# Kernel tuning notes

Hardware: AMD Instinct MI355X
Metric: run time of the kernel (lower is better)

Reference implementation:

```python
import jax, jax.numpy as jnp
import numpy as np

N_SRC, N_DST, DEG = 100000, 50000, 16
NODE_IN, EDGE_IN, HID = 128, 64, 64
E = N_DST * DEG


def sparsemax(z):
    # z: [..., K]; sparsemax along last axis (Martins & Astudillo)
    z = z - jnp.max(z, axis=-1, keepdims=True)
    zs = -jnp.sort(-z, axis=-1)  # descending sort
    k_range = jnp.arange(1, z.shape[-1] + 1, dtype=z.dtype)
    cs = jnp.cumsum(zs, axis=-1)
    is_gt = (1.0 + k_range * zs > cs).astype(z.dtype)
    k = jnp.max(is_gt * k_range, axis=-1, keepdims=True)
    tau = (jnp.sum(is_gt * zs, axis=-1, keepdims=True) - 1.0) / k
    return jnp.maximum(z - tau, 0.0)


def setup_inputs() -> dict:
    key = jax.random.key(0)
    ks = jax.random.split(key, 8)
    s = 0.02
    return {
        "node_features": jax.random.normal(ks[0], (N_SRC, NODE_IN), jnp.float32),
        "edge_features": jax.random.normal(ks[1], (E, EDGE_IN), jnp.float32),
        "src_idx": jax.random.randint(ks[2], (E,), 0, N_SRC, jnp.int32),
        "We": s * jax.random.normal(ks[3], (EDGE_IN, HID), jnp.float32),
        "be": jnp.zeros((HID,), jnp.float32),
        "Wa": s * jax.random.normal(ks[4], (EDGE_IN, HID), jnp.float32),
        "ba": jnp.zeros((HID,), jnp.float32),
        "wa": s * jax.random.normal(ks[5], (HID,), jnp.float32),
        "Wo": s * jax.random.normal(ks[6], (NODE_IN + HID, HID), jnp.float32),
        "bo": jnp.zeros((HID,), jnp.float32),
        "Wn": s * jax.random.normal(ks[7], (NODE_IN + HID, HID), jnp.float32),
        "bn": jnp.zeros((HID,), jnp.float32),
        "n_dst": N_DST,
        "deg": DEG,
    }


def reference(node_features, edge_features, src_idx, We, be, Wa, ba, wa, Wo, bo, Wn, bn, n_dst, deg):
    # dropout is identity in eval / p=0
    h_dst = node_features[:n_dst]                               # [n_dst, node_in]
    # message_func: per-edge transforms
    e_out = jax.nn.relu(edge_features @ We + be)                # [E, hid]
    a = jax.nn.leaky_relu((edge_features @ Wa + ba) @ wa)       # [E]
    h_src_e = node_features[src_idx]                            # gather [E, node_in]
    m = jax.nn.relu(jnp.concatenate([h_src_e, e_out], axis=-1) @ Wo + bo)  # [E, hid]
    # reduce_func: mailbox is [n_dst, deg, .] (fixed in-degree graph)
    a = a.reshape(n_dst, deg)
    m = m.reshape(n_dst, deg, -1)
    alpha = sparsemax(a)                                        # [n_dst, deg]
    h_neigh = jnp.einsum('nd,ndh->nh', alpha, m)                # [n_dst, hid]
    # node update
    return jax.nn.relu(jnp.concatenate([h_dst, h_neigh], axis=-1) @ Wn + bn)
```

## Files before the change

### kernel.cpp

```cpp
#include <hip/hip_runtime.h>


#define ND 50000
#define NS 100000

typedef __bf16 bf16x8 __attribute__((ext_vector_type(8)));
typedef float f32x4 __attribute__((ext_vector_type(4)));
typedef unsigned short u16x4 __attribute__((ext_vector_type(4)));

__device__ __forceinline__ void sync_wave() {
  asm volatile("s_waitcnt lgkmcnt(0)" ::: "memory");
}

__device__ __forceinline__ unsigned short f2bf(float x) {
  unsigned u = __float_as_uint(x);
  u += 0x7fffu + ((u >> 16) & 1u);
  return (unsigned short)(u >> 16);
}
__device__ __forceinline__ float bf2f(unsigned short u) {
  return __uint_as_float((unsigned)u << 16);
}

union Frag8 { bf16x8 v; unsigned u32[4]; };

__device__ __forceinline__ bf16x8 pack8(const float* fr) {
  Frag8 f;
  #pragma unroll
  for (int j = 0; j < 4; ++j) {
    unsigned lo = __float_as_uint(fr[2 * j]) + 0x8000u;
    unsigned hi = __float_as_uint(fr[2 * j + 1]) + 0x8000u;
    f.u32[j] = __builtin_amdgcn_perm(hi, lo, 0x07060302);
  }
  return f.v;
}

#define MFMA(a, b, c) __builtin_amdgcn_mfma_f32_16x16x32_bf16((a), (b), (c), 0, 0, 0)

extern "C" __global__ void gteast_prep(const float* __restrict__ Wa,
                                       const float* __restrict__ ba,
                                       const float* __restrict__ wa,
                                       float* __restrict__ vc) {
  __shared__ float red[260];
  const int tid = threadIdx.x, k = tid >> 2, p = tid & 3;
  float s = 0.f;
  for (int h = 16 * p; h < 16 * p + 16; ++h) s += Wa[k * 64 + h] * wa[h];
  red[tid] = s;
  if (tid < 4) {
    float sc = 0.f;
    for (int h = 16 * tid; h < 16 * tid + 16; ++h) sc += ba[h] * wa[h];
    red[256 + tid] = sc;
  }
  __syncthreads();
  if (p == 0) vc[k] = red[4 * k] + red[4 * k + 1] + red[4 * k + 2] + red[4 * k + 3];
  if (tid == 0) vc[64] = red[256] + red[257] + red[258] + red[259];
}

extern "C" __global__ void __launch_bounds__(256, 3)
gteast_src(const float* __restrict__ nf, const float* __restrict__ Wo,
           const float* __restrict__ Wn,
           unsigned short* __restrict__ y, unsigned short* __restrict__ z) {
  __shared__ unsigned short WuT[64 * 136];
  __shared__ unsigned short WnuT[64 * 136];
  const int tid = threadIdx.x;
  for (int i = tid; i < 128 * 64; i += 256) {
    int k = i >> 6, n = i & 63;
    WuT[n * 136 + k] = f2bf(Wo[i]);
    WnuT[n * 136 + k] = f2bf(Wn[i]);
  }
  __syncthreads();

  const int lane = tid & 63, w = tid >> 6, q = lane >> 4, t = lane & 15;
  const int tile = blockIdx.x * 4 + w;
  if (tile >= NS / 16) return;
  const int r0 = tile * 16;

  float raw[8];
  bf16x8 af[4];
  const float* hp = nf + (long)(r0 + t) * 128 + q * 8;
  #pragma unroll
  for (int kc = 0; kc < 4; ++kc) {
    float4 a0 = *reinterpret_cast<const float4*>(hp + kc * 32);
    float4 a1 = *reinterpret_cast<const float4*>(hp + kc * 32 + 4);
    raw[0] = a0.x; raw[1] = a0.y; raw[2] = a0.z; raw[3] = a0.w;
    raw[4] = a1.x; raw[5] = a1.y; raw[6] = a1.z; raw[7] = a1.w;
    af[kc] = pack8(raw);
  }

  f32x4 accY[4];
  #pragma unroll
  for (int nt = 0; nt < 4; ++nt) {
    f32x4 c = {0.f, 0.f, 0.f, 0.f};
    #pragma unroll
    for (int kc = 0; kc < 4; ++kc)
      c = MFMA(af[kc], *reinterpret_cast<const bf16x8*>(&WuT[(nt * 16 + t) * 136 + kc * 32 + q * 8]), c);
    accY[nt] = c;
  }
  #pragma unroll
  for (int r = 0; r < 4; ++r) {
    u16x4 v = {f2bf(accY[0][r]), f2bf(accY[1][r]), f2bf(accY[2][r]), f2bf(accY[3][r])};
    *reinterpret_cast<u16x4*>(y + (long)(r0 + 4 * q + r) * 64 + t * 4) = v;
  }

  if (tile < ND / 16) {
    f32x4 accZ[4];
    #pragma unroll
    for (int nt = 0; nt < 4; ++nt) {
      f32x4 c = {0.f, 0.f, 0.f, 0.f};
      #pragma unroll
      for (int kc = 0; kc < 4; ++kc)
        c = MFMA(af[kc], *reinterpret_cast<const bf16x8*>(&WnuT[(nt * 16 + t) * 136 + kc * 32 + q * 8]), c);
      accZ[nt] = c;
    }
    #pragma unroll
    for (int r = 0; r < 4; ++r) {
      u16x4 v = {f2bf(accZ[0][r]), f2bf(accZ[1][r]), f2bf(accZ[2][r]), f2bf(accZ[3][r])};
      *reinterpret_cast<u16x4*>(z + (long)(r0 + 4 * q + r) * 64 + t * 4) = v;
    }
  }
}

extern "C" __global__ void __launch_bounds__(256, 3)
gteast_edge(const float* __restrict__ ef, const int* __restrict__ src_idx,
            const float* __restrict__ We, const float* __restrict__ be,
            const float* __restrict__ Wo, const float* __restrict__ bo,
            const float* __restrict__ vc, const unsigned short* __restrict__ y,
            float* __restrict__ hn_out) {
  __shared__ unsigned short WeT[64 * 72];
  __shared__ unsigned short WoLoT[64 * 72];
  __shared__ unsigned short Elds[4][16 * 72];
  __shared__ float vls[68];

  const int tid = threadIdx.x;
  for (int i = tid; i < 64 * 64; i += 256) {
    int k = i >> 6, n = i & 63;
    WeT[n * 72 + k] = f2bf(We[i]);
  }
  for (int i = tid; i < 64 * 64; i += 256) {
    int k = i >> 6, n = i & 63;
    WoLoT[n * 72 + k] = f2bf(Wo[(128 + k) * 64 + n]);
  }
  if (tid < 65) vls[tid] = vc[tid];
  __syncthreads();

  const int lane = tid & 63, w = tid >> 6;
  const int q = lane >> 4, t = lane & 15;
  const int wid = blockIdx.x * 4 + w;
  if (wid * 8 >= ND) return;

  unsigned short* E = Elds[w];
  const float cval = vls[64];
  float beL[4], boL[4];
  #pragma unroll
  for (int nt = 0; nt < 4; ++nt) { beL[nt] = be[nt * 16 + t]; boL[nt] = bo[nt * 16 + t]; }
  float vsl[16];
  #pragma unroll
  for (int j = 0; j < 8; ++j) { vsl[j] = vls[q * 8 + j]; vsl[8 + j] = vls[32 + q * 8 + j]; }

  const int si0 = src_idx[wid * 128 + lane];
  const int si1 = src_idx[wid * 128 + 64 + lane];

  const long ebase = (long)(wid * 128);

  float4 efn[4];
  {
    const float* er = ef + (ebase + t) * 64 + q * 8;
    efn[0] = *reinterpret_cast<const float4*>(er);
    efn[1] = *reinterpret_cast<const float4*>(er + 4);
    efn[2] = *reinterpret_cast<const float4*>(er + 32);
    efn[3] = *reinterpret_cast<const float4*>(er + 36);
  }
  u16x4 yv[4];
  #pragma unroll
  for (int r = 0; r < 4; ++r) {
    const int s0 = __shfl(si0, 4 * q + r);
    yv[r] = *reinterpret_cast<const u16x4*>(y + (long)s0 * 64 + t * 4);
  }

  for (int it = 0; it < 8; ++it) {
    const int n = wid * 8 + it;
    const int itn = it < 7 ? it + 1 : 7;

    float fe[16];
    fe[0] = efn[0].x; fe[1] = efn[0].y; fe[2] = efn[0].z; fe[3] = efn[0].w;
    fe[4] = efn[1].x; fe[5] = efn[1].y; fe[6] = efn[1].z; fe[7] = efn[1].w;
    fe[8] = efn[2].x; fe[9] = efn[2].y; fe[10] = efn[2].z; fe[11] = efn[2].w;
    fe[12] = efn[3].x; fe[13] = efn[3].y; fe[14] = efn[3].z; fe[15] = efn[3].w;
    {
      const float* er = ef + (ebase + itn * 16 + t) * 64 + q * 8;
      efn[0] = *reinterpret_cast<const float4*>(er);
      efn[1] = *reinterpret_cast<const float4*>(er + 4);
      efn[2] = *reinterpret_cast<const float4*>(er + 32);
      efn[3] = *reinterpret_cast<const float4*>(er + 36);
    }

    float ap = 0.f;
    #pragma unroll
    for (int j = 0; j < 16; ++j) ap += fe[j] * vsl[j];
    ap += __shfl_xor(ap, 16);
    ap += __shfl_xor(ap, 32);
    float a = ap + cval;
    a = a > 0.f ? a : 0.01f * a;

    const bf16x8 e0 = pack8(fe), e1 = pack8(fe + 8);
    #pragma unroll
    for (int nt = 0; nt < 4; ++nt) {
      f32x4 c = {0.f, 0.f, 0.f, 0.f};
      c = MFMA(e0, *reinterpret_cast<const bf16x8*>(&WeT[(nt * 16 + t) * 72 + q * 8]), c);
      c = MFMA(e1, *reinterpret_cast<const bf16x8*>(&WeT[(nt * 16 + t) * 72 + 32 + q * 8]), c);
      #pragma unroll
      for (int r = 0; r < 4; ++r) {
        float vv = fmaxf(c[r] + beL[nt], 0.f);
        E[(4 * q + r) * 72 + nt * 16 + t] = f2bf(vv);
      }
    }
    sync_wave();

    bf16x8 af4 = *reinterpret_cast<const bf16x8*>(&E[t * 72 + q * 8]);
    bf16x8 af5 = *reinterpret_cast<const bf16x8*>(&E[t * 72 + 32 + q * 8]);

    f32x4 accM[4];
    #pragma unroll
    for (int nt = 0; nt < 4; ++nt) {
      f32x4 c = {0.f, 0.f, 0.f, 0.f};
      c = MFMA(af4, *reinterpret_cast<const bf16x8*>(&WoLoT[(nt * 16 + t) * 72 + q * 8]), c);
      c = MFMA(af5, *reinterpret_cast<const bf16x8*>(&WoLoT[(nt * 16 + t) * 72 + 32 + q * 8]), c);
      #pragma unroll
      for (int r = 0; r < 4; ++r)
        c[r] = fmaxf(c[r] + bf2f(yv[r][nt]) + boL[nt], 0.f);
      accM[nt] = c;
    }
    sync_wave();

    #pragma unroll
    for (int r = 0; r < 4; ++r) {
      const int idx = 16 * itn + 4 * q + r;
      const int sn = (idx < 64) ? __shfl(si0, idx) : __shfl(si1, idx - 64);
      yv[r] = *reinterpret_cast<const u16x4*>(y + (long)sn * 64 + t * 4);
    }

    const float z = a;
    float cp = 0.f, sp = 0.f;
    #pragma unroll
    for (int r = 0; r < 4; ++r) {
      float zj = __shfl(z, 4 * q + r, 16);
      const bool ge = (zj >= z);
      cp += ge ? 1.f : 0.f;
      sp += ge ? zj : 0.f;
    }
    cp += __shfl_xor(cp, 16); sp += __shfl_xor(sp, 16);
    cp += __shfl_xor(cp, 32); sp += __shfl_xor(sp, 32);
    const bool valid = 1.f + cp * z > sp;
    float kf = valid ? cp : 0.f;
    float sv = valid ? sp : 0.f;
    #pragma unroll
    for (int m = 1; m < 16; m <<= 1) {
      float ok = __shfl_xor(kf, m), os = __shfl_xor(sv, m);
      if (ok > kf) { kf = ok; sv = os; }
    }
    const float tau = (sv - 1.f) / kf;
    const float alpha = fmaxf(a - tau, 0.f);

    float al[4];
    #pragma unroll
    for (int r = 0; r < 4; ++r) al[r] = __shfl(alpha, 4 * q + r);
    float p[4];
    #pragma unroll
    for (int nt = 0; nt < 4; ++nt) {
      p[nt] = al[0] * accM[nt][0] + al[1] * accM[nt][1] +
              al[2] * accM[nt][2] + al[3] * accM[nt][3];
      p[nt] += __shfl_xor(p[nt], 16);
      p[nt] += __shfl_xor(p[nt], 32);
    }
    const float pown = (q == 0) ? p[0] : (q == 1) ? p[1] : (q == 2) ? p[2] : p[3];
    hn_out[(long)n * 64 + lane] = pown;
  }
}

extern "C" __global__ void __launch_bounds__(256, 4)
gteast_out(const unsigned short* __restrict__ z, const float* __restrict__ Wn,
           const float* __restrict__ bn, float* __restrict__ out) {
  __shared__ unsigned short WnLoT[64 * 72];
  const int tid = threadIdx.x;
  for (int i = tid; i < 64 * 64; i += 256) {
    int k = i >> 6, nn = i & 63;
    WnLoT[nn * 72 + k] = f2bf(Wn[(128 + k) * 64 + nn]);
  }
  __syncthreads();

  const int lane = tid & 63, w = tid >> 6, q = lane >> 4, t = lane & 15;
  const int tile = blockIdx.x * 4 + w;
  if (tile >= ND / 16) return;
  const int r0 = tile * 16;

  float bnL[4];
  #pragma unroll
  for (int nt = 0; nt < 4; ++nt) bnL[nt] = bn[nt * 16 + t];

  float raw[8];
  bf16x8 af4, af5;
  const float* gp = out + (long)(r0 + t) * 64 + q * 8;
  {
    float4 a0 = *reinterpret_cast<const float4*>(gp);
    float4 a1 = *reinterpret_cast<const float4*>(gp + 4);
    raw[0] = a0.x; raw[1] = a0.y; raw[2] = a0.z; raw[3] = a0.w;
    raw[4] = a1.x; raw[5] = a1.y; raw[6] = a1.z; raw[7] = a1.w;
    af4 = pack8(raw);
    a0 = *reinterpret_cast<const float4*>(gp + 32);
    a1 = *reinterpret_cast<const float4*>(gp + 36);
    raw[0] = a0.x; raw[1] = a0.y; raw[2] = a0.z; raw[3] = a0.w;
    raw[4] = a1.x; raw[5] = a1.y; raw[6] = a1.z; raw[7] = a1.w;
    af5 = pack8(raw);
  }
  u16x4 zv[4];
  #pragma unroll
  for (int r = 0; r < 4; ++r)
    zv[r] = *reinterpret_cast<const u16x4*>(z + (long)(r0 + 4 * q + r) * 64 + t * 4);

  #pragma unroll
  for (int nt = 0; nt < 4; ++nt) {
    f32x4 c = {0.f, 0.f, 0.f, 0.f};
    c = MFMA(af4, *reinterpret_cast<const bf16x8*>(&WnLoT[(nt * 16 + t) * 72 + q * 8]), c);
    c = MFMA(af5, *reinterpret_cast<const bf16x8*>(&WnLoT[(nt * 16 + t) * 72 + 32 + q * 8]), c);
    #pragma unroll
    for (int r = 0; r < 4; ++r)
      out[(long)(r0 + 4 * q + r) * 64 + nt * 16 + t] =
          fmaxf(c[r] + bf2f(zv[r][nt]) + bnL[nt], 0.f);
  }
}

extern "C" __global__ void __launch_bounds__(256, 3)
gteast_edge_fb(const float* __restrict__ nf, const float* __restrict__ ef,
               const int* __restrict__ src_idx,
               const float* __restrict__ We, const float* __restrict__ be,
               const float* __restrict__ Wo, const float* __restrict__ bo,
               const float* __restrict__ vc,
               float* __restrict__ hn_out) {
  __shared__ unsigned short WeT[64 * 72];
  __shared__ unsigned short WoT[64 * 200];
  __shared__ unsigned short Elds[4][16 * 72];
  __shared__ float vls[68];

  const int tid = threadIdx.x;
  for (int i = tid; i < 64 * 64; i += 256) {
    int k = i >> 6, n = i & 63;
    WeT[n * 72 + k] = f2bf(We[i]);
  }
  for (int i = tid; i < 192 * 64; i += 256) {
    int k = i >> 6, n = i & 63;
    WoT[n * 200 + k] = f2bf(Wo[i]);
  }
  if (tid < 65) vls[tid] = vc[tid];
  __syncthreads();

  const int lane = tid & 63, w = tid >> 6;
  const int q = lane >> 4, t = lane & 15;
  const int wid = blockIdx.x * 4 + w;
  if (wid * 8 >= ND) return;

  unsigned short* E = Elds[w];
  const float cval = vls[64];
  float beL[4], boL[4];
  #pragma unroll
  for (int nt = 0; nt < 4; ++nt) { beL[nt] = be[nt * 16 + t]; boL[nt] = bo[nt * 16 + t]; }
  float vsl[16];
  #pragma unroll
  for (int j = 0; j < 8; ++j) { vsl[j] = vls[q * 8 + j]; vsl[8 + j] = vls[32 + q * 8 + j]; }

  const int si0 = src_idx[wid * 128 + lane];
  const int si1 = src_idx[wid * 128 + 64 + lane];
  const long ebase = (long)(wid * 128);

  float4 efn[4];
  {
    const float* er = ef + (ebase + t) * 64 + q * 8;
    efn[0] = *reinterpret_cast<const float4*>(er);
    efn[1] = *reinterpret_cast<const float4*>(er + 4);
    efn[2] = *reinterpret_cast<const float4*>(er + 32);
    efn[3] = *reinterpret_cast<const float4*>(er + 36);
  }
  float hraw[32];
  {
    const int s0 = __shfl(si0, t);
    const float* hp = nf + (long)s0 * 128 + q * 8;
    #pragma unroll
    for (int kc = 0; kc < 4; ++kc) {
      float4 a0 = *reinterpret_cast<const float4*>(hp + kc * 32);
      float4 a1 = *reinterpret_cast<const float4*>(hp + kc * 32 + 4);
      hraw[kc * 8 + 0] = a0.x; hraw[kc * 8 + 1] = a0.y; hraw[kc * 8 + 2] = a0.z; hraw[kc * 8 + 3] = a0.w;
      hraw[kc * 8 + 4] = a1.x; hraw[kc * 8 + 5] = a1.y; hraw[kc * 8 + 6] = a1.z; hraw[kc * 8 + 7] = a1.w;
    }
  }

  for (int it = 0; it < 8; ++it) {
    const int n = wid * 8 + it;
    const int itn = it < 7 ? it + 1 : 7;

    float fe[16];
    fe[0] = efn[0].x; fe[1] = efn[0].y; fe[2] = efn[0].z; fe[3] = efn[0].w;
    fe[4] = efn[1].x; fe[5] = efn[1].y; fe[6] = efn[1].z; fe[7] = efn[1].w;
    fe[8] = efn[2].x; fe[9] = efn[2].y; fe[10] = efn[2].z; fe[11] = efn[2].w;
    fe[12] = efn[3].x; fe[13] = efn[3].y; fe[14] = efn[3].z; fe[15] = efn[3].w;
    {
      const float* er = ef + (ebase + itn * 16 + t) * 64 + q * 8;
      efn[0] = *reinterpret_cast<const float4*>(er);
      efn[1] = *reinterpret_cast<const float4*>(er + 4);
      efn[2] = *reinterpret_cast<const float4*>(er + 32);
      efn[3] = *reinterpret_cast<const float4*>(er + 36);
    }

    float ap = 0.f;
    #pragma unroll
    for (int j = 0; j < 16; ++j) ap += fe[j] * vsl[j];
    ap += __shfl_xor(ap, 16);
    ap += __shfl_xor(ap, 32);
    float a = ap + cval;
    a = a > 0.f ? a : 0.01f * a;

    const bf16x8 e0 = pack8(fe), e1 = pack8(fe + 8);
    #pragma unroll
    for (int nt = 0; nt < 4; ++nt) {
      f32x4 c = {0.f, 0.f, 0.f, 0.f};
      c = MFMA(e0, *reinterpret_cast<const bf16x8*>(&WeT[(nt * 16 + t) * 72 + q * 8]), c);
      c = MFMA(e1, *reinterpret_cast<const bf16x8*>(&WeT[(nt * 16 + t) * 72 + 32 + q * 8]), c);
      #pragma unroll
      for (int r = 0; r < 4; ++r) {
        float vv = fmaxf(c[r] + beL[nt], 0.f);
        E[(4 * q + r) * 72 + nt * 16 + t] = f2bf(vv);
      }
    }
    sync_wave();

    bf16x8 af[6];
    #pragma unroll
    for (int kc = 0; kc < 4; ++kc) af[kc] = pack8(hraw + kc * 8);
    af[4] = *reinterpret_cast<const bf16x8*>(&E[t * 72 + q * 8]);
    af[5] = *reinterpret_cast<const bf16x8*>(&E[t * 72 + 32 + q * 8]);

    {
      const int sn = (itn < 4) ? __shfl(si0, 16 * itn + t)
                               : __shfl(si1, 16 * (itn - 4) + t);
      const float* hp = nf + (long)sn * 128 + q * 8;
      #pragma unroll
      for (int kc = 0; kc < 4; ++kc) {
        float4 a0 = *reinterpret_cast<const float4*>(hp + kc * 32);
        float4 a1 = *reinterpret_cast<const float4*>(hp + kc * 32 + 4);
        hraw[kc * 8 + 0] = a0.x; hraw[kc * 8 + 1] = a0.y; hraw[kc * 8 + 2] = a0.z; hraw[kc * 8 + 3] = a0.w;
        hraw[kc * 8 + 4] = a1.x; hraw[kc * 8 + 5] = a1.y; hraw[kc * 8 + 6] = a1.z; hraw[kc * 8 + 7] = a1.w;
      }
    }

    f32x4 accM[4];
    #pragma unroll
    for (int nt = 0; nt < 4; ++nt) {
      f32x4 c = {0.f, 0.f, 0.f, 0.f};
      #pragma unroll
      for (int kc = 0; kc < 6; ++kc)
        c = MFMA(af[kc], *reinterpret_cast<const bf16x8*>(&WoT[(nt * 16 + t) * 200 + kc * 32 + q * 8]), c);
      #pragma unroll
      for (int r = 0; r < 4; ++r) c[r] = fmaxf(c[r] + boL[nt], 0.f);
      accM[nt] = c;
    }
    sync_wave();

    float zz = a;
    #pragma unroll
    for (int k = 2; k <= 16; k <<= 1) {
      #pragma unroll
      for (int j = k >> 1; j > 0; j >>= 1) {
        float o = __shfl_xor(zz, j);
        const bool upper = (t & j) != 0;
        const bool desc = (t & k) == 0;
        zz = (upper != desc) ? fmaxf(zz, o) : fminf(zz, o);
      }
    }
    float cs = zz;
    #pragma unroll
    for (int off = 1; off < 16; off <<= 1) {
      float o = __shfl_up(cs, off, 16);
      cs += (t >= off) ? o : 0.f;
    }
    const bool gt = 1.f + (float)(t + 1) * zz > cs;
    float kf = gt ? (float)(t + 1) : 0.f;
    float sv = gt ? zz : 0.f;
    #pragma unroll
    for (int m = 1; m < 16; m <<= 1) {
      kf = fmaxf(kf, __shfl_xor(kf, m));
      sv += __shfl_xor(sv, m);
    }
    const float tau = (sv - 1.f) / kf;
    const float alpha = fmaxf(a - tau, 0.f);

    float al[4];
    #pragma unroll
    for (int r = 0; r < 4; ++r) al[r] = __shfl(alpha, 4 * q + r);
    float p[4];
    #pragma unroll
    for (int nt = 0; nt < 4; ++nt) {
      p[nt] = al[0] * accM[nt][0] + al[1] * accM[nt][1] +
              al[2] * accM[nt][2] + al[3] * accM[nt][3];
      p[nt] += __shfl_xor(p[nt], 16);
      p[nt] += __shfl_xor(p[nt], 32);
    }
    const float pown = (q == 0) ? p[0] : (q == 1) ? p[1] : (q == 2) ? p[2] : p[3];
    hn_out[(long)n * 64 + lane] = pown;
  }
}

extern "C" __global__ void __launch_bounds__(256, 3)
gteast_out_fb(const float* __restrict__ nf, const float* __restrict__ Wn,
              const float* __restrict__ bn, float* __restrict__ out) {
  __shared__ unsigned short WnT[64 * 200];
  const int tid = threadIdx.x;
  for (int i = tid; i < 192 * 64; i += 256) {
    int k = i >> 6, nn = i & 63;
    WnT[nn * 200 + k] = f2bf(Wn[i]);
  }
  __syncthreads();

  const int lane = tid & 63, w = tid >> 6, q = lane >> 4, t = lane & 15;
  const int tile = blockIdx.x * 4 + w;
  if (tile >= ND / 16) return;
  const int r0 = tile * 16;

  float bnL[4];
  #pragma unroll
  for (int nt = 0; nt < 4; ++nt) bnL[nt] = bn[nt * 16 + t];

  float raw[8];
  bf16x8 af[6];
  const float* hp = nf + (long)(r0 + t) * 128 + q * 8;
  #pragma unroll
  for (int kc = 0; kc < 4; ++kc) {
    float4 a0 = *reinterpret_cast<const float4*>(hp + kc * 32);
    float4 a1 = *reinterpret_cast<const float4*>(hp + kc * 32 + 4);
    raw[0] = a0.x; raw[1] = a0.y; raw[2] = a0.z; raw[3] = a0.w;
    raw[4] = a1.x; raw[5] = a1.y; raw[6] = a1.z; raw[7] = a1.w;
    af[kc] = pack8(raw);
  }
  const float* gp = out + (long)(r0 + t) * 64 + q * 8;
  #pragma unroll
  for (int kc = 0; kc < 2; ++kc) {
    float4 a0 = *reinterpret_cast<const float4*>(gp + kc * 32);
    float4 a1 = *reinterpret_cast<const float4*>(gp + kc * 32 + 4);
    raw[0] = a0.x; raw[1] = a0.y; raw[2] = a0.z; raw[3] = a0.w;
    raw[4] = a1.x; raw[5] = a1.y; raw[6] = a1.z; raw[7] = a1.w;
    af[4 + kc] = pack8(raw);
  }

  #pragma unroll
  for (int nt = 0; nt < 4; ++nt) {
    f32x4 c = {0.f, 0.f, 0.f, 0.f};
    #pragma unroll
    for (int kc = 0; kc < 6; ++kc)
      c = MFMA(af[kc], *reinterpret_cast<const bf16x8*>(&WnT[(nt * 16 + t) * 200 + kc * 32 + q * 8]), c);
    #pragma unroll
    for (int r = 0; r < 4; ++r)
      out[(long)(r0 + 4 * q + r) * 64 + nt * 16 + t] = fmaxf(c[r] + bnL[nt], 0.f);
  }
}

extern "C" void kernel_launch(void* const* d_in, const int* in_sizes, int n_in,
                              void* d_out, int out_size, void* d_ws, size_t ws_size,
                              hipStream_t stream) {
  const float* nf = (const float*)d_in[0];
  const float* ef = (const float*)d_in[1];
  const int* si   = (const int*)d_in[2];
  const float* We = (const float*)d_in[3];
  const float* be = (const float*)d_in[4];
  const float* Wa = (const float*)d_in[5];
  const float* ba = (const float*)d_in[6];
  const float* wa = (const float*)d_in[7];
  const float* Wo = (const float*)d_in[8];
  const float* bo = (const float*)d_in[9];
  const float* Wn = (const float*)d_in[10];
  const float* bn = (const float*)d_in[11];
  float* out = (float*)d_out;
  float* vc = (float*)d_ws;

  const size_t yneed = 512 + (size_t)NS * 64 * 2 + (size_t)ND * 64 * 2;

  gteast_prep<<<1, 256, 0, stream>>>(Wa, ba, wa, vc);
  if (ws_size >= yneed) {
    unsigned short* y = (unsigned short*)((char*)d_ws + 512);
    unsigned short* z = y + (size_t)NS * 64;
    gteast_src<<<1563, 256, 0, stream>>>(nf, Wo, Wn, y, z);
    gteast_edge<<<1563, 256, 0, stream>>>(ef, si, We, be, Wo, bo, vc, y, out);
    gteast_out<<<782, 256, 0, stream>>>(z, Wn, bn, out);
  } else {
    gteast_edge_fb<<<1563, 256, 0, stream>>>(nf, ef, si, We, be, Wo, bo, vc, out);
    gteast_out_fb<<<782, 256, 0, stream>>>(nf, Wn, bn, out);
  }
}
```

Before: 370.0 us.

## Fold prep kernel into src launch, store hn as bf16, vectorize weight staging

Removes the separate prep launch by having an extra block of the src kernel compute the attention vector vc. The edge kernel now writes h_neigh as bf16 to a workspace buffer, which the output kernel loads directly as MFMA fragments instead of reading fp32 from out and packing it. Weight transposition into LDS now writes packed bf16 pairs as 32-bit stores, and the sparsemax tau search replaces the paired max/shuffle loop with a max reduction plus a ballot to pick the winning lane. The changes save a launch, halve the hn traffic and trim shuffles, at the cost of extra bf16 rounding of h_neigh and a larger workspace requirement.

```diff
diff --git a/kernel.cpp b/kernel.cpp
--- a/kernel.cpp
+++ b/kernel.cpp
@@ -19,6 +19,9 @@
 }
 __device__ __forceinline__ float bf2f(unsigned short u) {
   return __uint_as_float((unsigned)u << 16);
+}
+__device__ __forceinline__ unsigned f2bf2(float lo, float hi) {
+  return (unsigned)f2bf(lo) | ((unsigned)f2bf(hi) << 16);
 }
 
 union Frag8 { bf16x8 v; unsigned u32[4]; };
@@ -58,14 +61,37 @@
 extern "C" __global__ void __launch_bounds__(256, 3)
 gteast_src(const float* __restrict__ nf, const float* __restrict__ Wo,
            const float* __restrict__ Wn,
-           unsigned short* __restrict__ y, unsigned short* __restrict__ z) {
+           const float* __restrict__ Wa, const float* __restrict__ ba,
+           const float* __restrict__ wa,
+           unsigned short* __restrict__ y, unsigned short* __restrict__ z,
+           float* __restrict__ vc) {
   __shared__ unsigned short WuT[64 * 136];
   __shared__ unsigned short WnuT[64 * 136];
+  __shared__ float red[260];
   const int tid = threadIdx.x;
-  for (int i = tid; i < 128 * 64; i += 256) {
-    int k = i >> 6, n = i & 63;
-    WuT[n * 136 + k] = f2bf(Wo[i]);
-    WnuT[n * 136 + k] = f2bf(Wn[i]);
+
+  if (blockIdx.x == 1563) {
+    const int k = tid >> 2, p = tid & 3;
+    float s = 0.f;
+    for (int h = 16 * p; h < 16 * p + 16; ++h) s += Wa[k * 64 + h] * wa[h];
+    red[tid] = s;
+    if (tid < 4) {
+      float sc = 0.f;
+      for (int h = 16 * tid; h < 16 * tid + 16; ++h) sc += ba[h] * wa[h];
+      red[256 + tid] = sc;
+    }
+    __syncthreads();
+    if (p == 0) vc[k] = red[4 * k] + red[4 * k + 1] + red[4 * k + 2] + red[4 * k + 3];
+    if (tid == 0) vc[64] = red[256] + red[257] + red[258] + red[259];
+    return;
+  }
+
+  for (int i = tid; i < 64 * 64; i += 256) {
+    const int n = i & 63, k2 = i >> 6;
+    *reinterpret_cast<unsigned*>(&WuT[n * 136 + 2 * k2]) =
+        f2bf2(Wo[(2 * k2) * 64 + n], Wo[(2 * k2 + 1) * 64 + n]);
+    *reinterpret_cast<unsigned*>(&WnuT[n * 136 + 2 * k2]) =
+        f2bf2(Wn[(2 * k2) * 64 + n], Wn[(2 * k2 + 1) * 64 + n]);
   }
   __syncthreads();
 
@@ -124,20 +150,19 @@
             const float* __restrict__ We, const float* __restrict__ be,
             const float* __restrict__ Wo, const float* __restrict__ bo,
             const float* __restrict__ vc, const unsigned short* __restrict__ y,
-            float* __restrict__ hn_out) {
+            unsigned short* __restrict__ hn) {
   __shared__ unsigned short WeT[64 * 72];
   __shared__ unsigned short WoLoT[64 * 72];
   __shared__ unsigned short Elds[4][16 * 72];
   __shared__ float vls[68];
 
   const int tid = threadIdx.x;
-  for (int i = tid; i < 64 * 64; i += 256) {
-    int k = i >> 6, n = i & 63;
-    WeT[n * 72 + k] = f2bf(We[i]);
-  }
-  for (int i = tid; i < 64 * 64; i += 256) {
-    int k = i >> 6, n = i & 63;
-    WoLoT[n * 72 + k] = f2bf(Wo[(128 + k) * 64 + n]);
+  for (int i = tid; i < 64 * 32; i += 256) {
+    const int n = i & 63, k2 = i >> 6;
+    *reinterpret_cast<unsigned*>(&WeT[n * 72 + 2 * k2]) =
+        f2bf2(We[(2 * k2) * 64 + n], We[(2 * k2 + 1) * 64 + n]);
+    *reinterpret_cast<unsigned*>(&WoLoT[n * 72 + 2 * k2]) =
+        f2bf2(Wo[(128 + 2 * k2) * 64 + n], Wo[(129 + 2 * k2) * 64 + n]);
   }
   if (tid < 65) vls[tid] = vc[tid];
   __syncthreads();
@@ -238,26 +263,26 @@
       yv[r] = *reinterpret_cast<const u16x4*>(y + (long)sn * 64 + t * 4);
     }
 
-    const float z = a;
+    const float zz = a;
     float cp = 0.f, sp = 0.f;
     #pragma unroll
     for (int r = 0; r < 4; ++r) {
-      float zj = __shfl(z, 4 * q + r, 16);
-      const bool ge = (zj >= z);
+      float zj = __shfl(zz, 4 * q + r, 16);
+      const bool ge = (zj >= zz);
       cp += ge ? 1.f : 0.f;
       sp += ge ? zj : 0.f;
     }
     cp += __shfl_xor(cp, 16); sp += __shfl_xor(sp, 16);
     cp += __shfl_xor(cp, 32); sp += __shfl_xor(sp, 32);
-    const bool valid = 1.f + cp * z > sp;
+    const bool valid = 1.f + cp * zz > sp;
     float kf = valid ? cp : 0.f;
-    float sv = valid ? sp : 0.f;
-    #pragma unroll
-    for (int m = 1; m < 16; m <<= 1) {
-      float ok = __shfl_xor(kf, m), os = __shfl_xor(sv, m);
-      if (ok > kf) { kf = ok; sv = os; }
-    }
-    const float tau = (sv - 1.f) / kf;
+    #pragma unroll
+    for (int m = 1; m < 16; m <<= 1) kf = fmaxf(kf, __shfl_xor(kf, m));
+    const unsigned long long mk = __ballot(valid && (cp == kf));
+    const int base = lane & 48;
+    const int sl = __ffsll((unsigned long long)(mk >> base)) - 1 + base;
+    const float svm = __shfl(sp, sl);
+    const float tau = (svm - 1.f) / kf;
     const float alpha = fmaxf(a - tau, 0.f);
 
     float al[4];
@@ -272,18 +297,21 @@
       p[nt] += __shfl_xor(p[nt], 32);
     }
     const float pown = (q == 0) ? p[0] : (q == 1) ? p[1] : (q == 2) ? p[2] : p[3];
-    hn_out[(long)n * 64 + lane] = pown;
+    hn[(long)n * 64 + lane] = f2bf(pown);
   }
 }
 
 extern "C" __global__ void __launch_bounds__(256, 4)
-gteast_out(const unsigned short* __restrict__ z, const float* __restrict__ Wn,
+gteast_out(const unsigned short* __restrict__ z,
+           const unsigned short* __restrict__ hn,
+           const float* __restrict__ Wn,
            const float* __restrict__ bn, float* __restrict__ out) {
   __shared__ unsigned short WnLoT[64 * 72];
   const int tid = threadIdx.x;
-  for (int i = tid; i < 64 * 64; i += 256) {
-    int k = i >> 6, nn = i & 63;
-    WnLoT[nn * 72 + k] = f2bf(Wn[(128 + k) * 64 + nn]);
+  for (int i = tid; i < 64 * 32; i += 256) {
+    const int n = i & 63, k2 = i >> 6;
+    *reinterpret_cast<unsigned*>(&WnLoT[n * 72 + 2 * k2]) =
+        f2bf2(Wn[(128 + 2 * k2) * 64 + n], Wn[(129 + 2 * k2) * 64 + n]);
   }
   __syncthreads();
 
@@ -296,21 +324,10 @@
   #pragma unroll
   for (int nt = 0; nt < 4; ++nt) bnL[nt] = bn[nt * 16 + t];
 
-  float raw[8];
-  bf16x8 af4, af5;
-  const float* gp = out + (long)(r0 + t) * 64 + q * 8;
-  {
-    float4 a0 = *reinterpret_cast<const float4*>(gp);
-    float4 a1 = *reinterpret_cast<const float4*>(gp + 4);
-    raw[0] = a0.x; raw[1] = a0.y; raw[2] = a0.z; raw[3] = a0.w;
-    raw[4] = a1.x; raw[5] = a1.y; raw[6] = a1.z; raw[7] = a1.w;
-    af4 = pack8(raw);
-    a0 = *reinterpret_cast<const float4*>(gp + 32);
-    a1 = *reinterpret_cast<const float4*>(gp + 36);
-    raw[0] = a0.x; raw[1] = a0.y; raw[2] = a0.z; raw[3] = a0.w;
-    raw[4] = a1.x; raw[5] = a1.y; raw[6] = a1.z; raw[7] = a1.w;
-    af5 = pack8(raw);
-  }
+  const unsigned short* gp = hn + (long)(r0 + t) * 64 + q * 8;
+  const bf16x8 af4 = *reinterpret_cast<const bf16x8*>(gp);
+  const bf16x8 af5 = *reinterpret_cast<const bf16x8*>(gp + 32);
+
   u16x4 zv[4];
   #pragma unroll
   for (int r = 0; r < 4; ++r)
@@ -577,16 +594,17 @@
   float* out = (float*)d_out;
   float* vc = (float*)d_ws;
 
-  const size_t yneed = 512 + (size_t)NS * 64 * 2 + (size_t)ND * 64 * 2;
-
-  gteast_prep<<<1, 256, 0, stream>>>(Wa, ba, wa, vc);
+  const size_t yneed = 512 + (size_t)NS * 64 * 2 + (size_t)ND * 64 * 2 * 2;
+
   if (ws_size >= yneed) {
     unsigned short* y = (unsigned short*)((char*)d_ws + 512);
     unsigned short* z = y + (size_t)NS * 64;
-    gteast_src<<<1563, 256, 0, stream>>>(nf, Wo, Wn, y, z);
-    gteast_edge<<<1563, 256, 0, stream>>>(ef, si, We, be, Wo, bo, vc, y, out);
-    gteast_out<<<782, 256, 0, stream>>>(z, Wn, bn, out);
+    unsigned short* hn = z + (size_t)ND * 64;
+    gteast_src<<<1564, 256, 0, stream>>>(nf, Wo, Wn, Wa, ba, wa, y, z, vc);
+    gteast_edge<<<1563, 256, 0, stream>>>(ef, si, We, be, Wo, bo, vc, y, hn);
+    gteast_out<<<782, 256, 0, stream>>>(z, hn, Wn, bn, out);
   } else {
+    gteast_prep<<<1, 256, 0, stream>>>(Wa, ba, wa, vc);
     gteast_edge_fb<<<1563, 256, 0, stream>>>(nf, ef, si, We, be, Wo, bo, vc, out);
     gteast_out_fb<<<782, 256, 0, stream>>>(nf, Wn, bn, out);
   }
```

New measurement: 367.9 us. About the same (-0.6%).
